# Kernel optimization log

Hardware: AMD Instinct MI355X
Metric: run time of the kernel (lower is better)

Reference implementation:

```python
import jax, jax.numpy as jnp
import numpy as np

BIN_NUM = 20
BIN_WIDTH = 0.1
FEAT_MAP_NUM = 64


def setup_inputs() -> dict:
    key = jax.random.key(0)
    kx, kw, kb = jax.random.split(key, 3)
    B, C, H, W = 16, FEAT_MAP_NUM, 256, 256
    x = jax.random.normal(kx, (B, C, H, W), dtype=jnp.float32)
    # Faithful MTLU init: weight zeros for negative half-bins, ones for positive;
    # small noise added so the baseline exercises non-trivial per-bin values.
    half = BIN_NUM // 2
    w0 = jnp.concatenate(
        [jnp.zeros((C, half), jnp.float32), jnp.ones((C, BIN_NUM - half), jnp.float32)],
        axis=1,
    )
    mtluweight = w0 + 0.05 * jax.random.normal(kw, (C, BIN_NUM), dtype=jnp.float32)
    mtlubias = 0.05 * jax.random.normal(kb, (C, BIN_NUM), dtype=jnp.float32)
    return {"x": x, "mtluweight": mtluweight, "mtlubias": mtlubias}


def _mtlu(x, weight, bias):
    # per-element bin index: floor(x / BinWidth) + BinNum/2, clamped to [0, BinNum-1]
    idx = jnp.clip(
        jnp.floor(x * (1.0 / BIN_WIDTH)).astype(jnp.int32) + BIN_NUM // 2,
        0,
        BIN_NUM - 1,
    )  # [B,C,H,W] int32
    C = weight.shape[0]
    ch = jnp.arange(C, dtype=jnp.int32)[None, :, None, None]  # broadcast channel index
    w = weight[ch, idx]  # [B,C,H,W] gather per (channel, bin)
    b = bias[ch, idx]
    return w * x + b


def reference(x, mtluweight, mtlubias):
    tmp = _mtlu(x, mtluweight, mtlubias)
    return tmp * jax.nn.sigmoid(x)
```

## Files before the change

### kernel.cpp

```cpp
#include <hip/hip_runtime.h>
#include <hip/hip_bf16.h>


#define MT_C 64
#define MT_BINS 20
#define MT_TABLE (MT_C * MT_BINS)


__global__ __launch_bounds__(256) void mtsilu_kernel(
    const float4* __restrict__ x,
    const float* __restrict__ weight,
    const float* __restrict__ bias,
    float4* __restrict__ out,
    int nvec)
{
    __shared__ float sw[MT_TABLE];
    __shared__ float sb[MT_TABLE];
    for (int i = threadIdx.x; i < MT_TABLE; i += 256) {
        sw[i] = weight[i];
        sb[i] = bias[i];
    }
    __syncthreads();

    const int stride = gridDim.x * 256;
    for (int i = blockIdx.x * 256 + threadIdx.x; i < nvec; i += stride) {
        float4 v = x[i];
        const int cbase = ((i >> 14) & (MT_C - 1)) * MT_BINS;

        float r[4];
        float xv[4] = {v.x, v.y, v.z, v.w};
        #pragma unroll
        for (int k = 0; k < 4; ++k) {
            float xk = xv[k];
            int idx = (int)floorf(xk * 10.0f) + (MT_BINS / 2);
            idx = idx < 0 ? 0 : (idx > MT_BINS - 1 ? MT_BINS - 1 : idx);
            float wv = sw[cbase + idx];
            float bv = sb[cbase + idx];
            float s = 1.0f / (1.0f + __expf(-xk));
            r[k] = (wv * xk + bv) * s;
        }
        float4 o;
        o.x = r[0]; o.y = r[1]; o.z = r[2]; o.w = r[3];
        out[i] = o;
    }
}

extern "C" void kernel_launch(void* const* d_in, const int* in_sizes, int n_in,
                              void* d_out, int out_size, void* d_ws, size_t ws_size,
                              hipStream_t stream) {
    const float4* x      = (const float4*)d_in[0];
    const float*  weight = (const float*)d_in[1];
    const float*  bias   = (const float*)d_in[2];
    float4*       out    = (float4*)d_out;

    const int n    = in_sizes[0];
    const int nvec = n / 4;

    const int block = 256;
    const int grid  = 16384;
    mtsilu_kernel<<<grid, block, 0, stream>>>(x, weight, bias, out, nvec);
}
```

Before: 434.6 us.

## Unroll grid-stride loop, shrink grid, use fast reciprocal and uniform channel index

Cuts the grid from 16384 to 2048 blocks and unrolls the grid-stride loop four ways, issuing all four float4 loads before computing, so more memory requests are in flight and the per-block table-fill overhead shrinks. The channel base is computed with readfirstlane so it is treated as wave-uniform. Table fill now uses float4 copies, the sigmoid uses a hardware reciprocal, and the bin index uses round-down conversion with an fma. The readfirstlane relies on each wave staying inside one channel, which holds because the stride and block boundaries align to the 16384-vector channel size.

```diff
diff --git a/kernel.cpp b/kernel.cpp
--- a/kernel.cpp
+++ b/kernel.cpp
@@ -1,13 +1,25 @@
 #include <hip/hip_runtime.h>
-#include <hip/hip_bf16.h>
 
 
 #define MT_C 64
 #define MT_BINS 20
 #define MT_TABLE (MT_C * MT_BINS)
+#define NTHREADS 256
+#define NBLOCKS 2048
+#define UNROLL 4
 
+__device__ __forceinline__ float mtsilu_elem(float xk,
+                                             const float* __restrict__ swc,
+                                             const float* __restrict__ sbc) {
+    int idx = __float2int_rd(xk * 10.0f) + (MT_BINS / 2);
+    idx = idx < 0 ? 0 : (idx > MT_BINS - 1 ? MT_BINS - 1 : idx);
+    float wv = swc[idx];
+    float bv = sbc[idx];
+    float s = __builtin_amdgcn_rcpf(1.0f + __expf(-xk));
+    return fmaf(wv, xk, bv) * s;
+}
 
-__global__ __launch_bounds__(256) void mtsilu_kernel(
+__global__ __launch_bounds__(NTHREADS, 8) void mtsilu_kernel(
     const float4* __restrict__ x,
     const float* __restrict__ weight,
     const float* __restrict__ bias,
@@ -16,31 +28,51 @@
 {
     __shared__ float sw[MT_TABLE];
     __shared__ float sb[MT_TABLE];
-    for (int i = threadIdx.x; i < MT_TABLE; i += 256) {
-        sw[i] = weight[i];
-        sb[i] = bias[i];
+    {
+        const float4* w4 = (const float4*)weight;
+        const float4* b4 = (const float4*)bias;
+        float4* sw4 = (float4*)sw;
+        float4* sb4 = (float4*)sb;
+        for (int i = threadIdx.x; i < MT_TABLE / 4; i += NTHREADS) {
+            sw4[i] = w4[i];
+            sb4[i] = b4[i];
+        }
     }
     __syncthreads();
 
-    const int stride = gridDim.x * 256;
-    for (int i = blockIdx.x * 256 + threadIdx.x; i < nvec; i += stride) {
+    const int stride = gridDim.x * NTHREADS;
+    int i = (int)blockIdx.x * NTHREADS + (int)threadIdx.x;
+
+    for (; i + (UNROLL - 1) * stride < nvec; i += UNROLL * stride) {
+        float4 v[UNROLL];
+        int cb[UNROLL];
+        #pragma unroll
+        for (int u = 0; u < UNROLL; ++u) {
+            int j = i + u * stride;
+            v[u] = x[j];
+            int jc = __builtin_amdgcn_readfirstlane(j);
+            cb[u] = ((jc >> 14) & (MT_C - 1)) * MT_BINS;
+        }
+        #pragma unroll
+        for (int u = 0; u < UNROLL; ++u) {
+            const float* swc = sw + cb[u];
+            const float* sbc = sb + cb[u];
+            float4 o;
+            o.x = mtsilu_elem(v[u].x, swc, sbc);
+            o.y = mtsilu_elem(v[u].y, swc, sbc);
+            o.z = mtsilu_elem(v[u].z, swc, sbc);
+            o.w = mtsilu_elem(v[u].w, swc, sbc);
+            out[i + u * stride] = o;
+        }
+    }
+    for (; i < nvec; i += stride) {
         float4 v = x[i];
         const int cbase = ((i >> 14) & (MT_C - 1)) * MT_BINS;
-
-        float r[4];
-        float xv[4] = {v.x, v.y, v.z, v.w};
-        #pragma unroll
-        for (int k = 0; k < 4; ++k) {
-            float xk = xv[k];
-            int idx = (int)floorf(xk * 10.0f) + (MT_BINS / 2);
-            idx = idx < 0 ? 0 : (idx > MT_BINS - 1 ? MT_BINS - 1 : idx);
-            float wv = sw[cbase + idx];
-            float bv = sb[cbase + idx];
-            float s = 1.0f / (1.0f + __expf(-xk));
-            r[k] = (wv * xk + bv) * s;
-        }
         float4 o;
-        o.x = r[0]; o.y = r[1]; o.z = r[2]; o.w = r[3];
+        o.x = mtsilu_elem(v.x, sw + cbase, sb + cbase);
+        o.y = mtsilu_elem(v.y, sw + cbase, sb + cbase);
+        o.z = mtsilu_elem(v.z, sw + cbase, sb + cbase);
+        o.w = mtsilu_elem(v.w, sw + cbase, sb + cbase);
         out[i] = o;
     }
 }
@@ -56,7 +88,5 @@
     const int n    = in_sizes[0];
     const int nvec = n / 4;
 
-    const int block = 256;
-    const int grid  = 16384;
-    mtsilu_kernel<<<grid, block, 0, stream>>>(x, weight, bias, out, nvec);
+    mtsilu_kernel<<<NBLOCKS, NTHREADS, 0, stream>>>(x, weight, bias, out, nvec);
 }
```

Result: slower. 446.8 us (+2.8%).
